# Kernel tuning notes

Measured on AMD Instinct MI355X. Metric: run time of the kernel, lower is better.

Reference implementation:

```python
import jax, jax.numpy as jnp
import numpy as np

WS = 14          # window size (SAM ViT default)
NUM_HEADS = 12   # dim=768 -> head_dim=64
THETA = 10000.0  # rope theta


def _axial_rope_cos_sin(head_dim, end_x, end_y):
    # compute_axial_cis: head_dim//4 freqs per axis; t_x = t % end_x, t_y = t // end_x
    n = head_dim // 4
    freqs = 1.0 / (THETA ** (np.arange(0, head_dim, 4)[:n].astype(np.float32) / head_dim))
    t = np.arange(end_x * end_y, dtype=np.float32)
    t_x = t % end_x
    t_y = np.floor(t / end_x)
    ang = np.concatenate([t_x[:, None] * freqs[None, :], t_y[:, None] * freqs[None, :]], axis=-1)
    return jnp.asarray(np.cos(ang)), jnp.asarray(np.sin(ang))  # (N, head_dim//2) each


def _apply_rope(x, cos, sin):
    # x: (B, N, D) viewed as complex pairs along last dim (torch.view_as_complex ordering)
    x2 = x.reshape(x.shape[:-1] + (-1, 2))
    xr, xi = x2[..., 0], x2[..., 1]
    out_r = xr * cos - xi * sin
    out_i = xr * sin + xi * cos
    return jnp.stack([out_r, out_i], axis=-1).reshape(x.shape)


def setup_inputs() -> dict:
    key = jax.random.key(0)
    ks = jax.random.split(key, 6)
    B, H, W, C = 8, 64, 64, 768
    hd = C // NUM_HEADS
    max_rel = 2 * WS - 1
    return {
        "x": jax.random.normal(ks[0], (B, H, W, C), dtype=jnp.float32),
        "qkv_w": jax.random.normal(ks[1], (3 * C, C), dtype=jnp.float32) * 0.02,
        "qkv_b": jnp.zeros((3 * C,), dtype=jnp.float32),
        "proj_w": jax.random.normal(ks[2], (C, C), dtype=jnp.float32) * 0.02,
        "proj_b": jnp.zeros((C,), dtype=jnp.float32),
        "rel_pos_h": jax.random.normal(ks[3], (max_rel, hd), dtype=jnp.float32) * 0.02,
        "rel_pos_w": jax.random.normal(ks[4], (max_rel, hd), dtype=jnp.float32) * 0.02,
    }


def reference(x, qkv_w, qkv_b, proj_w, proj_b, rel_pos_h, rel_pos_w):
    B, H, W, C = x.shape
    nH = NUM_HEADS
    hd = C // nH
    N = WS * WS

    # --- window_partition with padding ---
    pad_h = (-H) % WS
    pad_w = (-W) % WS
    xp = jnp.pad(x, ((0, 0), (0, pad_h), (0, pad_w), (0, 0)))
    Hp, Wp = H + pad_h, W + pad_w
    nwh, nww = Hp // WS, Wp // WS
    xw = xp.reshape(B, nwh, WS, nww, WS, C).transpose(0, 1, 3, 2, 4, 5).reshape(-1, N, C)
    Bw = xw.shape[0]  # B * num_windows

    # --- qkv projection, split heads ---
    qkv = xw @ qkv_w.T + qkv_b                       # (Bw, N, 3C)
    qkv = qkv.reshape(Bw, N, 3, nH, hd).transpose(2, 0, 3, 1, 4).reshape(3, Bw * nH, N, hd)
    q, k, v = qkv[0], qkv[1], qkv[2]

    # --- 2D axial rotary encoding on q, k ---
    cos, sin = _axial_rope_cos_sin(hd, WS, WS)       # (N, hd//2)
    q = _apply_rope(q, cos, sin)
    k = _apply_rope(k, cos, sin)

    # --- decomposed relative-position bias (get_rel_pos gather + einsum) ---
    coords = jnp.arange(WS)[:, None] - jnp.arange(WS)[None, :] + (WS - 1)  # (WS, WS) in [0, 2WS-2]
    Rh = rel_pos_h[coords]                           # (WS, WS, hd)
    Rw = rel_pos_w[coords]
    r_q = q.reshape(-1, WS, WS, hd)
    rel_h = jnp.einsum('bhwc,hkc->bhwk', r_q, Rh)    # (BwnH, WS, WS, WS)
    rel_w = jnp.einsum('bhwc,wkc->bhwk', r_q, Rw)

    # --- attention: q k^T / sqrt(hd) + rel biases (math of concat_rel_pos + sdpa) ---
    attn = jnp.einsum('bqc,bkc->bqk', q, k) * (hd ** -0.5)
    attn = attn.reshape(-1, WS, WS, WS, WS) + rel_h[..., :, None] + rel_w[..., None, :]
    attn = jax.nn.softmax(attn.reshape(-1, N, N), axis=-1)
    out = attn @ v                                   # (BwnH, N, hd)

    # --- merge heads, output projection ---
    out = out.reshape(Bw, nH, WS, WS, hd).transpose(0, 2, 3, 1, 4).reshape(Bw, N, C)
    out = out @ proj_w.T + proj_b

    # --- window_unpartition, crop padding ---
    out = out.reshape(B, nwh, nww, WS, WS, C).transpose(0, 1, 3, 2, 4, 5).reshape(B, Hp, Wp, C)
    return out[:, :H, :W, :]
```

## Files before the change

### kernel.cpp

```cpp
#include <hip/hip_runtime.h>

using u16 = unsigned short;
using u32 = unsigned int;

typedef __bf16 bf16x8 __attribute__((ext_vector_type(8)));
typedef float f32x4 __attribute__((ext_vector_type(4)));

#define M32 32768

__device__ __forceinline__ u16 f2bf(float f) {
  u32 u = __float_as_uint(f);
  u += 0x7fffu + ((u >> 16) & 1u);
  return (u16)(u >> 16);
}
__device__ __forceinline__ u32 cvtpk(float a, float b) {
  u32 r; asm("v_cvt_pk_bf16_f32 %0, %1, %2" : "=v"(r) : "v"(a), "v"(b)); return r;
}
__device__ __forceinline__ float bflo(u32 w) { return __uint_as_float(w << 16); }
__device__ __forceinline__ float bfhi(u32 w) { return __uint_as_float(w & 0xffff0000u); }

__device__ __forceinline__ void async16(const void* g, void* l) {
  __builtin_amdgcn_global_load_lds((const __attribute__((address_space(1))) void*)g,
                                   (__attribute__((address_space(3))) void*)l, 16, 0, 0);
}

union frag { uint4 u; bf16x8 b; };

__global__ __launch_bounds__(256) void prep_w(const float* __restrict__ qw,
                                              const float* __restrict__ pw,
                                              u16* __restrict__ qwb, u16* __restrict__ pwb,
                                              float2* __restrict__ cs) {
  int i = blockIdx.x * 256 + threadIdx.x;
  if (i < 2304 * 768) qwb[i] = f2bf(qw[i]);
  if (i < 768 * 768)  pwb[i] = f2bf(pw[i]);
  if (i < 196 * 32) {
    int t = i >> 5, f = i & 31;
    float fr = powf(10000.f, -(float)(f & 15) * (1.f / 16.f));
    float ang = (f < 16 ? (float)(t % 14) : (float)(t / 14)) * fr;
    cs[i] = make_float2(cosf(ang), sinf(ang));
  }
}

template<int EPI>
__global__ __launch_bounds__(256) void gemm_bt(
    const void* __restrict__ Av, const u16* __restrict__ B,
    const float* __restrict__ bias, u16* __restrict__ Cb,
    float* __restrict__ Cf, int K, int N, int NTI)
{
  __shared__ u16 As[2][128 * 32];
  __shared__ u16 Bs[2][128 * 32];

  const int nwg = gridDim.x;
  const int orig = blockIdx.x;
  const int q = nwg >> 3, r = nwg & 7;
  const int xcd = orig & 7, loc = orig >> 3;
  const int wg = (xcd < r ? xcd * (q + 1) : r * (q + 1) + (xcd - r) * q) + loc;
  const int m0 = (wg / NTI) * 128;
  const int n0 = (wg % NTI) * 128;

  const int tid = threadIdx.x;
  const int lane = tid & 63;
  const int wv = tid >> 6;
  const int wm = wv >> 1, wn = wv & 1;
  const int lr = lane & 15, lq = lane >> 4;

  const int srow = tid >> 2, sg = (tid & 3) * 8;
  const float* Af0 = (const float*)Av + (size_t)(m0 + srow) * K + sg;
  const u16*   Ab0 = (const u16*)Av + (size_t)(m0 + srow) * K + sg;
  const u16*   B0  = B + (size_t)(n0 + srow) * K + sg;

  async16(B0, (void*)(Bs[0] + tid * 8));
  async16(B0 + (size_t)64 * K, (void*)(Bs[0] + 2048 + tid * 8));
  if constexpr (EPI == 0) {
    float4 a0 = *(const float4*)(Af0);
    float4 a1 = *(const float4*)(Af0 + 4);
    float4 a2 = *(const float4*)(Af0 + (size_t)64 * K);
    float4 a3 = *(const float4*)(Af0 + (size_t)64 * K + 4);
    *(uint4*)(As[0] + tid * 8) =
        make_uint4(cvtpk(a0.x, a0.y), cvtpk(a0.z, a0.w), cvtpk(a1.x, a1.y), cvtpk(a1.z, a1.w));
    *(uint4*)(As[0] + 2048 + tid * 8) =
        make_uint4(cvtpk(a2.x, a2.y), cvtpk(a2.z, a2.w), cvtpk(a3.x, a3.y), cvtpk(a3.z, a3.w));
  } else {
    async16(Ab0, (void*)(As[0] + tid * 8));
    async16(Ab0 + (size_t)64 * K, (void*)(As[0] + 2048 + tid * 8));
  }
  __syncthreads();

  f32x4 acc[4][4];
#pragma unroll
  for (int i = 0; i < 4; i++)
#pragma unroll
    for (int j = 0; j < 4; j++)
      acc[i][j] = f32x4{0.f, 0.f, 0.f, 0.f};

  const int NT = K / 32;
  for (int t = 0; t < NT; ++t) {
    const int cur = t & 1;
    const u16* Asc = As[cur];
    const u16* Bsc = Bs[cur];
    u16* Asn = As[cur ^ 1];
    u16* Bsn = Bs[cur ^ 1];
    const bool pre = (t + 1) < NT;
    const int k1 = (t + 1) * 32;

    float4 a0, a1, a2, a3;
    if (pre) {
      async16(B0 + k1, (void*)(Bsn + tid * 8));
      async16(B0 + (size_t)64 * K + k1, (void*)(Bsn + 2048 + tid * 8));
      if constexpr (EPI == 0) {
        a0 = *(const float4*)(Af0 + k1);
        a1 = *(const float4*)(Af0 + k1 + 4);
        a2 = *(const float4*)(Af0 + (size_t)64 * K + k1);
        a3 = *(const float4*)(Af0 + (size_t)64 * K + k1 + 4);
      } else {
        async16(Ab0 + k1, (void*)(Asn + tid * 8));
        async16(Ab0 + (size_t)64 * K + k1, (void*)(Asn + 2048 + tid * 8));
      }
    }

    frag af[4], bg[4];
#pragma unroll
    for (int i = 0; i < 4; i++) {
      af[i].u = *(const uint4*)(Asc + (wm * 64 + i * 16 + lr) * 32 + lq * 8);
      bg[i].u = *(const uint4*)(Bsc + (wn * 64 + i * 16 + lr) * 32 + lq * 8);
    }

    if (pre && EPI == 0) {
      *(uint4*)(Asn + tid * 8) =
          make_uint4(cvtpk(a0.x, a0.y), cvtpk(a0.z, a0.w), cvtpk(a1.x, a1.y), cvtpk(a1.z, a1.w));
      *(uint4*)(Asn + 2048 + tid * 8) =
          make_uint4(cvtpk(a2.x, a2.y), cvtpk(a2.z, a2.w), cvtpk(a3.x, a3.y), cvtpk(a3.z, a3.w));
    }

#pragma unroll
    for (int i = 0; i < 4; i++)
#pragma unroll
      for (int j = 0; j < 4; j++)
        acc[i][j] = __builtin_amdgcn_mfma_f32_16x16x32_bf16(af[i].b, bg[j].b, acc[i][j], 0, 0, 0);

    __syncthreads();
  }

#pragma unroll
  for (int i = 0; i < 4; i++) {
#pragma unroll
    for (int j = 0; j < 4; j++) {
      const int n = n0 + wn * 64 + j * 16 + lr;
      const int mb = m0 + wm * 64 + i * 16 + lq * 4;
      const float bv = bias[n];
#pragma unroll
      for (int rr = 0; rr < 4; rr++) {
        float val = acc[i][j][rr] + bv;
        int m = mb + rr;
        if (EPI == 0) Cb[(size_t)m * N + n] = f2bf(val);
        else          Cf[(size_t)m * N + n] = val;
      }
    }
  }
}

#define R1P 104
#define VTP 232
#define PQP 40
#define LDS_R1   (224 * R1P * 2)
#define LDS_VT   (64 * VTP * 2)
#define LDS_PB   (4 * 16 * PQP * 2)
#define LDS_TOT  (LDS_R1 + LDS_VT + LDS_PB)

__global__ __launch_bounds__(256, 2) void attn_mfma(
    const u16* __restrict__ qkv, u16* __restrict__ ao,
    const float* __restrict__ relph, const float* __restrict__ relpw,
    const float2* __restrict__ cs, const float* __restrict__ qb)
{
  extern __shared__ char smem[];
  u16*   R1  = (u16*)smem;
  u16*   VTb = (u16*)(smem + LDS_R1);
  u16*   Th  = VTb;
  u16*   Tw  = VTb + 256 * 28;
  char*  PBr = smem + LDS_R1 + LDS_VT;

  const int blk = blockIdx.x;
  const int w = blk / 12, h = blk % 12;
  const int tid = threadIdx.x;
  const int lane = tid & 63, wv = tid >> 6;
  const int lr = lane & 15, lq = lane >> 4;

  const int b0 = w / 25, rw_ = w % 25;
  const int wy = (rw_ / 5) * 14, wx = (rw_ % 5) * 14;
  const int ty = tid / 14, tx = tid - ty * 14;
  const int gh = wy + ty, gw = wx + tx;
  const bool inb = (tid < 196) && (gh < 64) && (gw < 64);
  const size_t grow = (size_t)((b0 * 64 + gh) * 64 + gw);

  {
    float qf[64];
    if (tid < 196) {
      if (inb) {
        const u16* qp = qkv + grow * 2304 + h * 64;
        uint4 q4[8];
#pragma unroll
        for (int u = 0; u < 8; u++) q4[u] = *(const uint4*)(qp + u * 8);
#pragma unroll
        for (int u = 0; u < 8; u++) {
          qf[u*8+0] = bflo(q4[u].x); qf[u*8+1] = bfhi(q4[u].x);
          qf[u*8+2] = bflo(q4[u].y); qf[u*8+3] = bfhi(q4[u].y);
          qf[u*8+4] = bflo(q4[u].z); qf[u*8+5] = bfhi(q4[u].z);
          qf[u*8+6] = bflo(q4[u].w); qf[u*8+7] = bfhi(q4[u].w);
        }
      } else {
        const float4* bp = (const float4*)(qb + h * 64);
#pragma unroll
        for (int u = 0; u < 16; u++) {
          float4 t4 = bp[u];
          qf[u*4+0] = t4.x; qf[u*4+1] = t4.y; qf[u*4+2] = t4.z; qf[u*4+3] = t4.w;
        }
      }
      const float2* ct = cs + tid * 32;
#pragma unroll
      for (int f = 0; f < 32; f++) {
        float2 c2 = ct[f];
        float xr = qf[2*f], xi = qf[2*f+1];
        qf[2*f]   = (xr * c2.x - xi * c2.y) * 0.125f;
        qf[2*f+1] = (xr * c2.y + xi * c2.x) * 0.125f;
      }
    } else {
#pragma unroll
      for (int d = 0; d < 64; d++) qf[d] = 0.f;
    }
    if (tid < 224) {
      u16* dst = R1 + tid * R1P;
#pragma unroll
      for (int u = 0; u < 8; u++)
        *(uint4*)(dst + u * 8) = make_uint4(cvtpk(qf[u*8+0], qf[u*8+1]), cvtpk(qf[u*8+2], qf[u*8+3]),
                                            cvtpk(qf[u*8+4], qf[u*8+5]), cvtpk(qf[u*8+6], qf[u*8+7]));
    }
  }

  uint4 k4[8], v4[8];
  if (inb) {
    const u16* kp = qkv + grow * 2304 + 768 + h * 64;
    const u16* vp = qkv + grow * 2304 + 1536 + h * 64;
#pragma unroll
    for (int u = 0; u < 8; u++) k4[u] = *(const uint4*)(kp + u * 8);
#pragma unroll
    for (int u = 0; u < 8; u++) v4[u] = *(const uint4*)(vp + u * 8);
  }
  __syncthreads();

  frag af[4][3];
#pragma unroll
  for (int i = 0; i < 4; i++)
#pragma unroll
    for (int kc = 0; kc < 2; kc++) {
      if (wv == 3 && i >= 2)
        af[i][kc].u = make_uint4(0u, 0u, 0u, 0u);
      else
        af[i][kc].u = *(const uint4*)(R1 + (wv * 64 + i * 16 + lr) * R1P + kc * 32 + lq * 8);
    }

#pragma unroll
  for (int n = 0; n < 2; n++) {
    f32x4 tah[4], taw[4];
#pragma unroll
    for (int i = 0; i < 4; i++) { tah[i] = f32x4{0,0,0,0}; taw[i] = f32x4{0,0,0,0}; }
    const int j = n * 16 + lr;
#pragma unroll
    for (int kc = 0; kc < 2; kc++) {
      float4 ha = {0,0,0,0}, hb = {0,0,0,0}, wa = {0,0,0,0}, wb2 = {0,0,0,0};
      if (j < 27) {
        const float* ph  = relph + j * 64 + kc * 32 + lq * 8;
        const float* pw2 = relpw + j * 64 + kc * 32 + lq * 8;
        ha = *(const float4*)ph;  hb  = *(const float4*)(ph + 4);
        wa = *(const float4*)pw2; wb2 = *(const float4*)(pw2 + 4);
      }
      frag bh, bw;
      bh.u = make_uint4(cvtpk(ha.x, ha.y), cvtpk(ha.z, ha.w), cvtpk(hb.x, hb.y), cvtpk(hb.z, hb.w));
      bw.u = make_uint4(cvtpk(wa.x, wa.y), cvtpk(wa.z, wa.w), cvtpk(wb2.x, wb2.y), cvtpk(wb2.z, wb2.w));
#pragma unroll
      for (int i = 0; i < 4; i++) {
        tah[i] = __builtin_amdgcn_mfma_f32_16x16x32_bf16(af[i][kc].b, bh.b, tah[i], 0, 0, 0);
        taw[i] = __builtin_amdgcn_mfma_f32_16x16x32_bf16(af[i][kc].b, bw.b, taw[i], 0, 0, 0);
      }
    }
    int jcol = n * 16 + lr;
    if (jcol < 28) {
#pragma unroll
      for (int i = 0; i < 4; i++)
#pragma unroll
        for (int r2 = 0; r2 < 4; r2++) {
          int qq = wv * 64 + i * 16 + lq * 4 + r2;
          Th[qq * 28 + jcol] = f2bf(tah[i][r2] * 8.f);
          Tw[qq * 28 + jcol] = f2bf(taw[i][r2] * 8.f);
        }
    }
  }
  __syncthreads();

  {
    u32 wb[16];
#pragma unroll
    for (int z = 0; z < 16; z++) wb[z] = 0;
    if (tid < 196) {
      const u16* thr = Th + tid * 28 + ty + 13;
      const u16* twr = Tw + tid * 28 + tx + 13;
#pragma unroll
      for (int p = 0; p < 7; p++) wb[p]     = (u32)thr[-(2*p)] | ((u32)thr[-(2*p+1)] << 16);
#pragma unroll
      for (int p = 0; p < 7; p++) wb[7 + p] = (u32)twr[-(2*p)] | ((u32)twr[-(2*p+1)] << 16);
    }
    wb[14] = 0xC1F0u;
    if (tid < 224) {
      u16* dst = R1 + tid * R1P + 64;
#pragma unroll
      for (int u = 0; u < 4; u++)
        *(uint4*)(dst + u * 8) = make_uint4(wb[u*4], wb[u*4+1], wb[u*4+2], wb[u*4+3]);
    }
  }
  __syncthreads();

#pragma unroll
  for (int i = 0; i < 4; i++) {
    if (wv == 3 && i >= 2)
      af[i][2].u = make_uint4(0u, 0u, 0u, 0u);
    else
      af[i][2].u = *(const uint4*)(R1 + (wv * 64 + i * 16 + lr) * R1P + 64 + lq * 8);
  }
  __syncthreads();

  if (tid < 224) {
    const bool real = tid < 196;
    u32 kw[32];
#pragma unroll
    for (int z = 0; z < 32; z++) kw[z] = 0;
    if (real) {
      float kf[64];
      if (inb) {
#pragma unroll
        for (int u = 0; u < 8; u++) {
          kf[u*8+0] = bflo(k4[u].x); kf[u*8+1] = bfhi(k4[u].x);
          kf[u*8+2] = bflo(k4[u].y); kf[u*8+3] = bfhi(k4[u].y);
          kf[u*8+4] = bflo(k4[u].z); kf[u*8+5] = bfhi(k4[u].z);
          kf[u*8+6] = bflo(k4[u].w); kf[u*8+7] = bfhi(k4[u].w);
        }
      } else {
        const float4* bp = (const float4*)(qb + 768 + h * 64);
#pragma unroll
        for (int u = 0; u < 16; u++) {
          float4 t4 = bp[u];
          kf[u*4+0] = t4.x; kf[u*4+1] = t4.y; kf[u*4+2] = t4.z; kf[u*4+3] = t4.w;
        }
      }
      const float2* ct = cs + tid * 32;
#pragma unroll
      for (int f = 0; f < 32; f++) {
        float2 c2 = ct[f];
        float xr = kf[2*f], xi = kf[2*f+1];
        kf[2*f]   = xr * c2.x - xi * c2.y;
        kf[2*f+1] = xr * c2.y + xi * c2.x;
      }
#pragma unroll
      for (int p = 0; p < 32; p++) kw[p] = cvtpk(kf[2*p], kf[2*p+1]);
    }
    const int tA = real ? 64 + ty : 92;
    const int tB = real ? 78 + tx : 92;
    u32 aw[16];
#pragma unroll
    for (int p = 0; p < 16; p++) {
      const int c0 = 64 + 2 * p, c1 = c0 + 1;
      u32 lo = (c0 == tA || c0 == tB) ? 0x3F80u : 0u;
      u32 hi = (c1 == tA || c1 == tB) ? 0x3F80u : 0u;
      aw[p] = lo | (hi << 16);
    }
    u16* dst = R1 + tid * R1P;
#pragma unroll
    for (int u = 0; u < 8; u++)
      *(uint4*)(dst + u * 8) = make_uint4(kw[u*4], kw[u*4+1], kw[u*4+2], kw[u*4+3]);
#pragma unroll
    for (int u = 0; u < 4; u++)
      *(uint4*)(dst + 64 + u * 8) = make_uint4(aw[u*4], aw[u*4+1], aw[u*4+2], aw[u*4+3]);

    if (real) {
      u16* col = VTb + tid;
      if (inb) {
#pragma unroll
        for (int u = 0; u < 8; u++) {
          col[(u*8+0) * VTP] = (u16)(v4[u].x & 0xffff); col[(u*8+1) * VTP] = (u16)(v4[u].x >> 16);
          col[(u*8+2) * VTP] = (u16)(v4[u].y & 0xffff); col[(u*8+3) * VTP] = (u16)(v4[u].y >> 16);
          col[(u*8+4) * VTP] = (u16)(v4[u].z & 0xffff); col[(u*8+5) * VTP] = (u16)(v4[u].z >> 16);
          col[(u*8+6) * VTP] = (u16)(v4[u].w & 0xffff); col[(u*8+7) * VTP] = (u16)(v4[u].w >> 16);
        }
      } else {
        const float4* bp = (const float4*)(qb + 1536 + h * 64);
#pragma unroll
        for (int u = 0; u < 16; u++) {
          float4 t4 = bp[u];
          col[(u*4+0) * VTP] = f2bf(t4.x); col[(u*4+1) * VTP] = f2bf(t4.y);
          col[(u*4+2) * VTP] = f2bf(t4.z); col[(u*4+3) * VTP] = f2bf(t4.w);
        }
      }
    } else {
#pragma unroll
      for (int d = 0; d < 64; d++) VTb[d * VTP + tid] = 0;
    }
  }
  __syncthreads();

  f32x4 oacc[4][4];
  f32x4 lacc[4];
#pragma unroll
  for (int i = 0; i < 4; i++) {
    lacc[i] = f32x4{0,0,0,0};
#pragma unroll
    for (int j = 0; j < 4; j++) oacc[i][j] = f32x4{0,0,0,0};
  }
  frag ones;
  ones.u = make_uint4(0x3F803F80u, 0x3F803F80u, 0x3F803F80u, 0x3F803F80u);
  u16* PB = (u16*)PBr + wv * 16 * PQP;

  for (int c = 0; c < 7; c++) {
    frag bk[2][3];
#pragma unroll
    for (int kt = 0; kt < 2; kt++)
#pragma unroll
      for (int kc = 0; kc < 3; kc++)
        bk[kt][kc].u = *(const uint4*)(R1 + (c * 32 + kt * 16 + lr) * R1P + kc * 32 + lq * 8);

    frag bv[4];
#pragma unroll
    for (int j = 0; j < 4; j++)
      bv[j].u = *(const uint4*)(VTb + (j * 16 + lr) * VTP + c * 32 + lq * 8);

    f32x4 sacc[4][2];
#pragma unroll
    for (int i = 0; i < 4; i++) { sacc[i][0] = f32x4{0,0,0,0}; sacc[i][1] = f32x4{0,0,0,0}; }
#pragma unroll
    for (int kc = 0; kc < 3; kc++)
#pragma unroll
      for (int i = 0; i < 4; i++)
#pragma unroll
        for (int kt = 0; kt < 2; kt++)
          sacc[i][kt] = __builtin_amdgcn_mfma_f32_16x16x32_bf16(af[i][kc].b, bk[kt][kc].b, sacc[i][kt], 0, 0, 0);

#pragma unroll
    for (int i = 0; i < 4; i++) {
#pragma unroll
      for (int kt = 0; kt < 2; kt++)
#pragma unroll
        for (int r2 = 0; r2 < 4; r2++)
          PB[(lq * 4 + r2) * PQP + kt * 16 + lr] = f2bf(__expf(sacc[i][kt][r2]));

      frag pf;
      pf.u = *(const uint4*)(PB + lr * PQP + lq * 8);

      lacc[i] = __builtin_amdgcn_mfma_f32_16x16x32_bf16(pf.b, ones.b, lacc[i], 0, 0, 0);
#pragma unroll
      for (int j = 0; j < 4; j++)
        oacc[i][j] = __builtin_amdgcn_mfma_f32_16x16x32_bf16(pf.b, bv[j].b, oacc[i][j], 0, 0, 0);
    }
  }

#pragma unroll
  for (int i = 0; i < 4; i++) {
    f32x4 inv;
#pragma unroll
    for (int r2 = 0; r2 < 4; r2++) inv[r2] = 1.f / lacc[i][r2];
#pragma unroll
    for (int r2 = 0; r2 < 4; r2++) {
      int qq = wv * 64 + i * 16 + lq * 4 + r2;
      if (qq < 196) {
        int qy = qq / 14, qx = qq - qy * 14;
        int gh2 = wy + qy, gw2 = wx + qx;
        if (gh2 < 64 && gw2 < 64) {
          u16* op = ao + (size_t)((b0 * 64 + gh2) * 64 + gw2) * 768 + h * 64 + lr;
#pragma unroll
          for (int j = 0; j < 4; j++)
            op[j * 16] = f2bf(oacc[i][j][r2] * inv[r2]);
        }
      }
    }
  }
}

extern "C" void kernel_launch(void* const* d_in, const int* in_sizes, int n_in,
                              void* d_out, int out_size, void* d_ws, size_t ws_size,
                              hipStream_t stream) {
  const float* x      = (const float*)d_in[0];
  const float* qkv_w  = (const float*)d_in[1];
  const float* qkv_b  = (const float*)d_in[2];
  const float* proj_w = (const float*)d_in[3];
  const float* proj_b = (const float*)d_in[4];
  const float* rel_h  = (const float*)d_in[5];
  const float* rel_w  = (const float*)d_in[6];
  float* out = (float*)d_out;

  char* ws = (char*)d_ws;
  u16* qkvb = (u16*)ws;
  u16* ao   = (u16*)(ws + (size_t)M32 * 2304 * 2);
  u16* qwb  = (u16*)(ws + (size_t)M32 * 2304 * 2 + (size_t)M32 * 768 * 2);
  u16* pwb  = qwb + 2304 * 768;
  float2* cs = (float2*)(pwb + 768 * 768);

  prep_w<<<6912, 256, 0, stream>>>(qkv_w, proj_w, qwb, pwb, cs);
  gemm_bt<0><<<dim3(256 * 18), 256, 0, stream>>>(x, qwb, qkv_b, qkvb, nullptr, 768, 2304, 18);
  attn_mfma<<<2400, 256, LDS_TOT, stream>>>(qkvb, ao, rel_h, rel_w, cs, qkv_b);
  gemm_bt<1><<<dim3(256 * 6), 256, 0, stream>>>(ao, pwb, proj_b, nullptr, out, 768, 768, 6);
}
```

Before: 540.7 us.

## Swizzle GEMM LDS tiles, remap attention blocks per XCD, use exp2 softmax

The GEMM's shared-memory layout for A and B tiles now uses an XOR swizzle in both the staging stores and the fragment reads, aimed at reducing LDS bank conflicts. The fp32-to-bf16 store of the next A tile is moved after the MFMA loop so it overlaps with compute. The attention kernel remaps block indices so consecutive windows and heads land on the same XCD, for better L2 locality. It also folds log2(e) into the q scale and the mask constant so the native exp2 instruction replaces __expf. The swizzle must match exactly between the async B/A loads, which still write to tid*8, and the fragment read offsets. Any mismatch there would silently corrupt results.

```diff
diff --git a/kernel.cpp b/kernel.cpp
--- a/kernel.cpp
+++ b/kernel.cpp
@@ -18,6 +18,14 @@
 }
 __device__ __forceinline__ float bflo(u32 w) { return __uint_as_float(w << 16); }
 __device__ __forceinline__ float bfhi(u32 w) { return __uint_as_float(w & 0xffff0000u); }
+
+__device__ __forceinline__ float exp2h(float x) {
+#if __has_builtin(__builtin_amdgcn_exp2f)
+  return __builtin_amdgcn_exp2f(x);
+#else
+  float e; asm("v_exp_f32 %0, %1\n\ts_nop 0" : "=v"(e) : "v"(x)); return e;
+#endif
+}
 
 __device__ __forceinline__ void async16(const void* g, void* l) {
   __builtin_amdgcn_global_load_lds((const __attribute__((address_space(1))) void*)g,
@@ -64,10 +72,15 @@
   const int wm = wv >> 1, wn = wv & 1;
   const int lr = lane & 15, lq = lane >> 4;
 
-  const int srow = tid >> 2, sg = (tid & 3) * 8;
-  const float* Af0 = (const float*)Av + (size_t)(m0 + srow) * K + sg;
-  const u16*   Ab0 = (const u16*)Av + (size_t)(m0 + srow) * K + sg;
-  const u16*   B0  = B + (size_t)(n0 + srow) * K + sg;
+  const int srow0 = ((tid >> 6) << 4) + ((tid >> 2) & 15);
+  const int sgsw  = ((tid & 3) ^ (((tid >> 5) & 1) << 1)) * 8;
+  const u16* B0 = B + (size_t)(n0 + srow0) * K + sgsw;
+  const u16* Ab0 = (const u16*)Av + (size_t)(m0 + srow0) * K + sgsw;
+  const float* Af0 = (const float*)Av + (size_t)(m0 + (tid >> 2)) * K + (tid & 3) * 8;
+  const int dA = (((tid >> 6) * 64) + ((tid >> 2) & 15) * 4 +
+                  ((tid & 3) ^ (((tid >> 5) & 1) << 1))) * 8;
+
+  const int fro = lr * 32 + ((lq ^ (((lr >> 3) & 1) << 1)) << 3);
 
   async16(B0, (void*)(Bs[0] + tid * 8));
   async16(B0 + (size_t)64 * K, (void*)(Bs[0] + 2048 + tid * 8));
@@ -76,9 +89,9 @@
     float4 a1 = *(const float4*)(Af0 + 4);
     float4 a2 = *(const float4*)(Af0 + (size_t)64 * K);
     float4 a3 = *(const float4*)(Af0 + (size_t)64 * K + 4);
-    *(uint4*)(As[0] + tid * 8) =
+    *(uint4*)(As[0] + dA) =
         make_uint4(cvtpk(a0.x, a0.y), cvtpk(a0.z, a0.w), cvtpk(a1.x, a1.y), cvtpk(a1.z, a1.w));
-    *(uint4*)(As[0] + 2048 + tid * 8) =
+    *(uint4*)(As[0] + 2048 + dA) =
         make_uint4(cvtpk(a2.x, a2.y), cvtpk(a2.z, a2.w), cvtpk(a3.x, a3.y), cvtpk(a3.z, a3.w));
   } else {
     async16(Ab0, (void*)(As[0] + tid * 8));
@@ -121,15 +134,8 @@
     frag af[4], bg[4];
 #pragma unroll
     for (int i = 0; i < 4; i++) {
-      af[i].u = *(const uint4*)(Asc + (wm * 64 + i * 16 + lr) * 32 + lq * 8);
-      bg[i].u = *(const uint4*)(Bsc + (wn * 64 + i * 16 + lr) * 32 + lq * 8);
-    }
-
-    if (pre && EPI == 0) {
-      *(uint4*)(Asn + tid * 8) =
-          make_uint4(cvtpk(a0.x, a0.y), cvtpk(a0.z, a0.w), cvtpk(a1.x, a1.y), cvtpk(a1.z, a1.w));
-      *(uint4*)(Asn + 2048 + tid * 8) =
-          make_uint4(cvtpk(a2.x, a2.y), cvtpk(a2.z, a2.w), cvtpk(a3.x, a3.y), cvtpk(a3.z, a3.w));
+      af[i].u = *(const uint4*)(Asc + (wm * 4 + i) * 512 + fro);
+      bg[i].u = *(const uint4*)(Bsc + (wn * 4 + i) * 512 + fro);
     }
 
 #pragma unroll
@@ -137,6 +143,13 @@
 #pragma unroll
       for (int j = 0; j < 4; j++)
         acc[i][j] = __builtin_amdgcn_mfma_f32_16x16x32_bf16(af[i].b, bg[j].b, acc[i][j], 0, 0, 0);
+
+    if (pre && EPI == 0) {
+      *(uint4*)(Asn + dA) =
+          make_uint4(cvtpk(a0.x, a0.y), cvtpk(a0.z, a0.w), cvtpk(a1.x, a1.y), cvtpk(a1.z, a1.w));
+      *(uint4*)(Asn + 2048 + dA) =
+          make_uint4(cvtpk(a2.x, a2.y), cvtpk(a2.z, a2.w), cvtpk(a3.x, a3.y), cvtpk(a3.z, a3.w));
+    }
 
     __syncthreads();
   }
@@ -179,7 +192,8 @@
   u16*   Tw  = VTb + 256 * 28;
   char*  PBr = smem + LDS_R1 + LDS_VT;
 
-  const int blk = blockIdx.x;
+  const int orig = blockIdx.x;
+  const int blk = (orig & 7) * 300 + (orig >> 3);
   const int w = blk / 12, h = blk % 12;
   const int tid = threadIdx.x;
   const int lane = tid & 63, wv = tid >> 6;
@@ -220,8 +234,8 @@
       for (int f = 0; f < 32; f++) {
         float2 c2 = ct[f];
         float xr = qf[2*f], xi = qf[2*f+1];
-        qf[2*f]   = (xr * c2.x - xi * c2.y) * 0.125f;
-        qf[2*f+1] = (xr * c2.y + xi * c2.x) * 0.125f;
+        qf[2*f]   = (xr * c2.x - xi * c2.y) * 0.18033688f;
+        qf[2*f+1] = (xr * c2.y + xi * c2.x) * 0.18033688f;
       }
     } else {
 #pragma unroll
@@ -308,7 +322,7 @@
 #pragma unroll
       for (int p = 0; p < 7; p++) wb[7 + p] = (u32)twr[-(2*p)] | ((u32)twr[-(2*p+1)] << 16);
     }
-    wb[14] = 0xC1F0u;
+    wb[14] = 0xC22Du;
     if (tid < 224) {
       u16* dst = R1 + tid * R1P + 64;
 #pragma unroll
@@ -447,7 +461,7 @@
       for (int kt = 0; kt < 2; kt++)
 #pragma unroll
         for (int r2 = 0; r2 < 4; r2++)
-          PB[(lq * 4 + r2) * PQP + kt * 16 + lr] = f2bf(__expf(sacc[i][kt][r2]));
+          PB[(lq * 4 + r2) * PQP + kt * 16 + lr] = f2bf(exp2h(sacc[i][kt][r2]));
 
       frag pf;
       pf.u = *(const uint4*)(PB + lr * PQP + lq * 8);
```

Measured after the change: 541.6 us. Within noise of the previous version (+0.2%).
